# Optimization experiments

Measured on AMD Instinct MI355X. Metric: run time of the kernel, lower is better.

Reference implementation:

```python
import jax, jax.numpy as jnp
import numpy as np

B, IN, H, OUT, E = 4096, 1024, 2048, 1024, 16

def setup_inputs() -> dict:
    key = jax.random.key(0)
    ks = jax.random.split(key, 8)
    def lin_init(k, shape, fan_in):
        bound = 1.0 / np.sqrt(fan_in)
        return jax.random.uniform(k, shape, jnp.float32, -bound, bound)
    return {
        "obs": jax.random.normal(ks[0], (B, IN), jnp.float32),
        "switch_idx": jax.random.randint(ks[1], (B,), 0, E, jnp.int32),
        "pre_w": lin_init(ks[2], (H, IN), IN),
        "pre_b": lin_init(ks[3], (H,), IN),
        "expert_w": lin_init(ks[4], (E, H, H), H),
        "expert_b": lin_init(ks[5], (E, H), H),
        "post_w": lin_init(ks[6], (OUT, H), H),
        "post_b": lin_init(ks[7], (OUT,), H),
    }

def reference(obs, switch_idx, pre_w, pre_b, expert_w, expert_b, post_w, post_b):
    # pre_switch: Linear + Tanh
    x = jnp.tanh(obs @ pre_w.T + pre_b)                      # [B, H]
    # compute ALL switch experts (faithful to torch.stack over switches)
    all_x = jnp.einsum("bi,eoi->beo", x, expert_w) + expert_b  # [B, E, H]
    # gather the selected expert output per sample
    x = jnp.take_along_axis(all_x, switch_idx[:, None, None].astype(jnp.int32), axis=1)[:, 0]  # [B, H]
    # post_switch: Tanh, Linear, Tanh
    x = jnp.tanh(x)
    return jnp.tanh(x @ post_w.T + post_b)                   # [B, OUT]
```

## Files before the change

### kernel.cpp

```cpp
#include <hip/hip_runtime.h>


#define Bsz 4096
#define INd 1024
#define Hd  2048
#define OUTd 1024
#define NEXP 16

#define BM 128
#define BN 128
#define BK 32
#define LDT 56

typedef short bf16x8 __attribute__((ext_vector_type(8)));
typedef float f32x4 __attribute__((ext_vector_type(4)));
typedef unsigned short u16;

__device__ __forceinline__ u16 f2bf(float f) {
  unsigned u = __float_as_uint(f);
  u += 0x7FFF + ((u >> 16) & 1);
  return (u16)(u >> 16);
}

__device__ __forceinline__ float fast_tanh(float x) {
  float ax = fabsf(x);
  float e = __expf(2.0f * ax);
  float t = 1.0f - 2.0f / (e + 1.0f);
  return x < 0.0f ? -t : t;
}

__device__ __forceinline__ void mfma_step(const u16* As, const u16* Bs,
                                          int wm, int wn, int fr, int fk,
                                          f32x4 acc[4][4]) {
  bf16x8 af[4], bq[4];
#pragma unroll
  for (int i = 0; i < 4; ++i) af[i] = *(const bf16x8*)&As[(wm + 16 * i + fr) * LDT + fk];
#pragma unroll
  for (int j = 0; j < 4; ++j) bq[j] = *(const bf16x8*)&Bs[(wn + 16 * j + fr) * LDT + fk];
#pragma unroll
  for (int i = 0; i < 4; ++i)
#pragma unroll
    for (int j = 0; j < 4; ++j)
      acc[i][j] = __builtin_amdgcn_mfma_f32_16x16x32_bf16(af[i], bq[j], acc[i][j], 0, 0, 0);
}

__global__ __launch_bounds__(256) void k_bucket(const int* __restrict__ idx,
                                                int* __restrict__ offs,
                                                int* __restrict__ rows) {
  __shared__ int cnt[NEXP];
  __shared__ int base[NEXP];
  int t = threadIdx.x;
  if (t < NEXP) cnt[t] = 0;
  __syncthreads();
  for (int b = t; b < Bsz; b += 256) atomicAdd(&cnt[idx[b]], 1);
  __syncthreads();
  if (t == 0) {
    int s = 0;
    for (int e = 0; e < NEXP; ++e) { base[e] = s; offs[e] = s; s += cnt[e]; }
    offs[NEXP] = s;
  }
  __syncthreads();
  for (int b = t; b < Bsz; b += 256) {
    int e = idx[b];
    int p = atomicAdd(&base[e], 1);
    rows[p] = b;
  }
}

__global__ __launch_bounds__(256) void k_pre(const float* __restrict__ obs,
                                             const float* __restrict__ pre_w,
                                             const float* __restrict__ pre_b,
                                             u16* __restrict__ X1) {
  __shared__ u16 As[BM * LDT];
  __shared__ u16 Bs[BN * LDT];
  const int n0 = blockIdx.x * BN;
  const int m0 = blockIdx.y * BM;
  const int tid = threadIdx.x;
  const int lane = tid & 63;
  const int wv = tid >> 6;
  const int wm = (wv >> 1) * 64, wn = (wv & 1) * 64;
  const int fr = lane & 15, fq = lane >> 4;
  const int fk = fq * 8;
  const int sr = tid >> 3;
  const int skc = (tid & 7) * 4;

  f32x4 acc[4][4] = {};

  for (int k0 = 0; k0 < INd; k0 += BK) {
#pragma unroll
    for (int p = 0; p < 4; ++p) {
      int row = sr + 32 * p;
      float4 va = *(const float4*)&obs[(size_t)(m0 + row) * INd + k0 + skc];
      ushort4 ha; ha.x = f2bf(va.x); ha.y = f2bf(va.y); ha.z = f2bf(va.z); ha.w = f2bf(va.w);
      *(ushort4*)&As[row * LDT + skc] = ha;
      float4 vb = *(const float4*)&pre_w[(size_t)(n0 + row) * INd + k0 + skc];
      ushort4 hb; hb.x = f2bf(vb.x); hb.y = f2bf(vb.y); hb.z = f2bf(vb.z); hb.w = f2bf(vb.w);
      *(ushort4*)&Bs[row * LDT + skc] = hb;
    }
    __syncthreads();
    mfma_step(As, Bs, wm, wn, fr, fk, acc);
    __syncthreads();
  }
#pragma unroll
  for (int j = 0; j < 4; ++j) {
    int col = n0 + wn + 16 * j + fr;
    float bias = pre_b[col];
#pragma unroll
    for (int i = 0; i < 4; ++i) {
      int rb = m0 + wm + 16 * i + fq * 4;
#pragma unroll
      for (int r = 0; r < 4; ++r)
        X1[(size_t)(rb + r) * Hd + col] = f2bf(fast_tanh(acc[i][j][r] + bias));
    }
  }
}

__global__ __launch_bounds__(256) void k_expert(const u16* __restrict__ X1,
                                                const float* __restrict__ ew,
                                                const float* __restrict__ eb,
                                                const int* __restrict__ offs,
                                                const int* __restrict__ rows,
                                                u16* __restrict__ Z) {
  __shared__ u16 As[BM * LDT];
  __shared__ u16 Bs[BN * LDT];
  const int e = blockIdx.y >> 5;
  const int rt = blockIdx.y & 31;
  const int seg = offs[e];
  const int cnt = offs[e + 1] - seg;
  const int tbase = rt * BM;
  if (tbase >= cnt) return;
  const int nval = min(BM, cnt - tbase);
  const int n0 = blockIdx.x * BN;
  const float* We = ew + (size_t)e * Hd * Hd;

  const int tid = threadIdx.x;
  const int lane = tid & 63;
  const int wv = tid >> 6;
  const int wm = (wv >> 1) * 64, wn = (wv & 1) * 64;
  const int fr = lane & 15, fq = lane >> 4;
  const int fk = fq * 8;

  const int ar_ = tid >> 2;
  const int akc = (tid & 3) * 8;
  int rowg[2];
#pragma unroll
  for (int p = 0; p < 2; ++p) {
    int ar = ar_ + 64 * p;
    rowg[p] = (ar < nval) ? rows[seg + tbase + ar] : -1;
  }
  const int sr = tid >> 3;
  const int skc = (tid & 7) * 4;

  f32x4 acc[4][4] = {};
  const float4 zero4 = {0.f, 0.f, 0.f, 0.f};

  for (int k0 = 0; k0 < Hd; k0 += BK) {
#pragma unroll
    for (int p = 0; p < 2; ++p) {
      int ar = ar_ + 64 * p;
      float4 v = (rowg[p] >= 0) ? *(const float4*)&X1[(size_t)rowg[p] * Hd + k0 + akc] : zero4;
      *(float4*)&As[ar * LDT + akc] = v;
    }
#pragma unroll
    for (int p = 0; p < 4; ++p) {
      int row = sr + 32 * p;
      float4 vb = *(const float4*)&We[(size_t)(n0 + row) * Hd + k0 + skc];
      ushort4 hb; hb.x = f2bf(vb.x); hb.y = f2bf(vb.y); hb.z = f2bf(vb.z); hb.w = f2bf(vb.w);
      *(ushort4*)&Bs[row * LDT + skc] = hb;
    }
    __syncthreads();
    mfma_step(As, Bs, wm, wn, fr, fk, acc);
    __syncthreads();
  }
#pragma unroll
  for (int i = 0; i < 4; ++i) {
#pragma unroll
    for (int r = 0; r < 4; ++r) {
      int arow = wm + 16 * i + fq * 4 + r;
      if (arow < nval) {
        int orow = rows[seg + tbase + arow];
#pragma unroll
        for (int j = 0; j < 4; ++j) {
          int col = n0 + wn + 16 * j + fr;
          float bias = eb[(size_t)e * Hd + col];
          Z[(size_t)orow * Hd + col] = f2bf(fast_tanh(acc[i][j][r] + bias));
        }
      }
    }
  }
}

__global__ __launch_bounds__(256) void k_post(const u16* __restrict__ Z,
                                              const float* __restrict__ pw,
                                              const float* __restrict__ pb,
                                              float* __restrict__ out) {
  __shared__ u16 As[BM * LDT];
  __shared__ u16 Bs[BN * LDT];
  const int n0 = blockIdx.x * BN;
  const int m0 = blockIdx.y * BM;
  const int tid = threadIdx.x;
  const int lane = tid & 63;
  const int wv = tid >> 6;
  const int wm = (wv >> 1) * 64, wn = (wv & 1) * 64;
  const int fr = lane & 15, fq = lane >> 4;
  const int fk = fq * 8;
  const int ar_ = tid >> 2;
  const int akc = (tid & 3) * 8;
  const int sr = tid >> 3;
  const int skc = (tid & 7) * 4;

  f32x4 acc[4][4] = {};

  for (int k0 = 0; k0 < Hd; k0 += BK) {
#pragma unroll
    for (int p = 0; p < 2; ++p) {
      int ar = ar_ + 64 * p;
      float4 v = *(const float4*)&Z[(size_t)(m0 + ar) * Hd + k0 + akc];
      *(float4*)&As[ar * LDT + akc] = v;
    }
#pragma unroll
    for (int p = 0; p < 4; ++p) {
      int row = sr + 32 * p;
      float4 vb = *(const float4*)&pw[(size_t)(n0 + row) * Hd + k0 + skc];
      ushort4 hb; hb.x = f2bf(vb.x); hb.y = f2bf(vb.y); hb.z = f2bf(vb.z); hb.w = f2bf(vb.w);
      *(ushort4*)&Bs[row * LDT + skc] = hb;
    }
    __syncthreads();
    mfma_step(As, Bs, wm, wn, fr, fk, acc);
    __syncthreads();
  }
#pragma unroll
  for (int j = 0; j < 4; ++j) {
    int col = n0 + wn + 16 * j + fr;
    float bias = pb[col];
#pragma unroll
    for (int i = 0; i < 4; ++i) {
      int rb = m0 + wm + 16 * i + fq * 4;
#pragma unroll
      for (int r = 0; r < 4; ++r)
        out[(size_t)(rb + r) * OUTd + col] = fast_tanh(acc[i][j][r] + bias);
    }
  }
}

extern "C" void kernel_launch(void* const* d_in, const int* in_sizes, int n_in,
                              void* d_out, int out_size, void* d_ws, size_t ws_size,
                              hipStream_t stream) {
  const float* obs   = (const float*)d_in[0];
  const int*   sw    = (const int*)d_in[1];
  const float* pre_w = (const float*)d_in[2];
  const float* pre_b = (const float*)d_in[3];
  const float* ew    = (const float*)d_in[4];
  const float* eb    = (const float*)d_in[5];
  const float* pw    = (const float*)d_in[6];
  const float* pb    = (const float*)d_in[7];
  float* out = (float*)d_out;

  char* ws = (char*)d_ws;
  u16* X1   = (u16*)ws;
  u16* Z    = (u16*)(ws + (size_t)Bsz * Hd * 2);
  int* offs = (int*)(ws + (size_t)2 * Bsz * Hd * 2);
  int* rows = offs + 32;

  k_bucket<<<dim3(1), dim3(256), 0, stream>>>(sw, offs, rows);
  k_pre<<<dim3(Hd / BN, Bsz / BM), dim3(256), 0, stream>>>(obs, pre_w, pre_b, X1);
  k_expert<<<dim3(Hd / BN, NEXP * 32), dim3(256), 0, stream>>>(X1, ew, eb, offs, rows, Z);
  k_post<<<dim3(OUTd / BN, Bsz / BM), dim3(256), 0, stream>>>(Z, pw, pb, out);
}
```

Measured before the change: 649.6 us.

## Rewrite GEMM pipeline with bf16 pre-conversion, direct-to-LDS loads and double buffering

Adds conversion kernels that turn obs and the weights into bf16 in workspace, so the GEMMs stream bf16 through global_load_lds into XOR-swizzled, double-buffered LDS tiles with BK=64. A register-prefetch fallback runs when the workspace is too small. The post GEMM moves to 64-row tiles for more blocks. This removes per-tile fp32-to-bf16 conversion from the inner loops and overlaps loads with MFMA, at the cost of extra conversion passes over all weights (including 256MB of expert weights) on every call.

```diff
diff --git a/kernel.cpp b/kernel.cpp
--- a/kernel.cpp
+++ b/kernel.cpp
@@ -7,11 +7,6 @@
 #define OUTd 1024
 #define NEXP 16
 
-#define BM 128
-#define BN 128
-#define BK 32
-#define LDT 56
-
 typedef short bf16x8 __attribute__((ext_vector_type(8)));
 typedef float f32x4 __attribute__((ext_vector_type(4)));
 typedef unsigned short u16;
@@ -29,27 +24,88 @@
   return x < 0.0f ? -t : t;
 }
 
-__device__ __forceinline__ void mfma_step(const u16* As, const u16* Bs,
-                                          int wm, int wn, int fr, int fk,
-                                          f32x4 acc[4][4]) {
-  bf16x8 af[4], bq[4];
-#pragma unroll
-  for (int i = 0; i < 4; ++i) af[i] = *(const bf16x8*)&As[(wm + 16 * i + fr) * LDT + fk];
-#pragma unroll
-  for (int j = 0; j < 4; ++j) bq[j] = *(const bf16x8*)&Bs[(wn + 16 * j + fr) * LDT + fk];
-#pragma unroll
-  for (int i = 0; i < 4; ++i)
-#pragma unroll
-    for (int j = 0; j < 4; ++j)
-      acc[i][j] = __builtin_amdgcn_mfma_f32_16x16x32_bf16(af[i], bq[j], acc[i][j], 0, 0, 0);
+#define GLL16(g, l)                                                            \
+  __builtin_amdgcn_global_load_lds(                                            \
+      (const __attribute__((address_space(1))) unsigned int*)(g),              \
+      (__attribute__((address_space(3))) unsigned int*)(l), 16, 0, 0)
+
+__device__ __forceinline__ void stage128(const u16* gbase, int ldk, u16* lds, int t) {
+  const int row = t >> 3;
+  const int gc8 = ((t & 7) ^ (row & 7)) << 3;
+#pragma unroll
+  for (int p = 0; p < 4; ++p)
+    GLL16(gbase + (size_t)(row + 32 * p) * ldk + gc8, lds + ((t + 256 * p) << 3));
+}
+
+__device__ __forceinline__ void stage64(const u16* gbase, int ldk, u16* lds, int t) {
+  const int row = t >> 3;
+  const int gc8 = ((t & 7) ^ (row & 7)) << 3;
+#pragma unroll
+  for (int p = 0; p < 2; ++p)
+    GLL16(gbase + (size_t)(row + 32 * p) * ldk + gc8, lds + ((t + 256 * p) << 3));
+}
+
+__device__ __forceinline__ void stage_gather(const u16* X1k, const int rowg[4],
+                                             const u16* zeroc, u16* lds, int t) {
+  const int gc8 = ((t & 7) ^ ((t >> 3) & 7)) << 3;
+#pragma unroll
+  for (int p = 0; p < 4; ++p) {
+    const u16* g = (rowg[p] >= 0) ? X1k + (size_t)rowg[p] * Hd + gc8 : zeroc;
+    GLL16(g, lds + ((t + 256 * p) << 3));
+  }
+}
+
+struct F32Tile { float4 v[8]; };
+__device__ __forceinline__ void loadF32tile(const float* W, int ldk, int t, F32Tile& r) {
+  const int brow = t & 127, half = t >> 7;
+  const float* p = W + (size_t)brow * ldk + (half << 5);
+#pragma unroll
+  for (int q = 0; q < 8; ++q) r.v[q] = *(const float4*)(p + 4 * q);
+}
+__device__ __forceinline__ void writeF32tile(const F32Tile& r, u16* lds, int t) {
+  const int brow = t & 127, half = t >> 7;
+#pragma unroll
+  for (int q2 = 0; q2 < 4; ++q2) {
+    const float4 x = r.v[2 * q2], y = r.v[2 * q2 + 1];
+    bf16x8 o;
+    o[0] = (short)f2bf(x.x); o[1] = (short)f2bf(x.y);
+    o[2] = (short)f2bf(x.z); o[3] = (short)f2bf(x.w);
+    o[4] = (short)f2bf(y.x); o[5] = (short)f2bf(y.y);
+    o[6] = (short)f2bf(y.z); o[7] = (short)f2bf(y.w);
+    const int gq = (half << 2) + q2;
+    const int c = gq ^ (brow & 7);
+    *(bf16x8*)&lds[brow * 64 + (c << 3)] = o;
+  }
+}
+
+template <int MI>
+__device__ __forceinline__ void compute_tile(const u16* As, const u16* Bs,
+                                             int wm, int wn, int fr, int fq,
+                                             f32x4 (&acc)[MI][4]) {
+#pragma unroll
+  for (int ks = 0; ks < 2; ++ks) {
+    const int ch = (((ks << 2) + fq) ^ (fr & 7)) << 3;
+    bf16x8 af[MI], bq[4];
+#pragma unroll
+    for (int i = 0; i < MI; ++i) af[i] = *(const bf16x8*)&As[(wm + 16 * i + fr) * 64 + ch];
+#pragma unroll
+    for (int j = 0; j < 4; ++j) bq[j] = *(const bf16x8*)&Bs[(wn + 16 * j + fr) * 64 + ch];
+#pragma unroll
+    for (int i = 0; i < MI; ++i)
+#pragma unroll
+      for (int j = 0; j < 4; ++j)
+        acc[i][j] = __builtin_amdgcn_mfma_f32_16x16x32_bf16(af[i], bq[j], acc[i][j], 0, 0, 0);
+  }
 }
 
 __global__ __launch_bounds__(256) void k_bucket(const int* __restrict__ idx,
                                                 int* __restrict__ offs,
-                                                int* __restrict__ rows) {
+                                                int* __restrict__ rows,
+                                                int* __restrict__ zc) {
   __shared__ int cnt[NEXP];
   __shared__ int base[NEXP];
   int t = threadIdx.x;
+  if (t < 16) zc[t] = 0;
   if (t < NEXP) cnt[t] = 0;
   __syncthreads();
   for (int b = t; b < Bsz; b += 256) atomicAdd(&cnt[idx[b]], 1);
@@ -67,111 +123,155 @@
   }
 }
 
-__global__ __launch_bounds__(256) void k_pre(const float* __restrict__ obs,
-                                             const float* __restrict__ pre_w,
-                                             const float* __restrict__ pre_b,
-                                             u16* __restrict__ X1) {
-  __shared__ u16 As[BM * LDT];
-  __shared__ u16 Bs[BN * LDT];
-  const int n0 = blockIdx.x * BN;
-  const int m0 = blockIdx.y * BM;
-  const int tid = threadIdx.x;
-  const int lane = tid & 63;
-  const int wv = tid >> 6;
-  const int wm = (wv >> 1) * 64, wn = (wv & 1) * 64;
+__global__ __launch_bounds__(256) void k_cvt(const float* __restrict__ src,
+                                             u16* __restrict__ dst, int n) {
+  int i = (blockIdx.x * 256 + threadIdx.x) * 8;
+  if (i >= n) return;
+  float4 a = *(const float4*)(src + i);
+  float4 b = *(const float4*)(src + i + 4);
+  bf16x8 o;
+  o[0] = (short)f2bf(a.x); o[1] = (short)f2bf(a.y);
+  o[2] = (short)f2bf(a.z); o[3] = (short)f2bf(a.w);
+  o[4] = (short)f2bf(b.x); o[5] = (short)f2bf(b.y);
+  o[6] = (short)f2bf(b.z); o[7] = (short)f2bf(b.w);
+  *(bf16x8*)(dst + i) = o;
+}
+
+template <bool PC>
+__global__ __launch_bounds__(256) void k_pre_t(const float* __restrict__ obs32,
+                                               const u16* __restrict__ obsb,
+                                               const float* __restrict__ prew32,
+                                               const u16* __restrict__ prewb,
+                                               const float* __restrict__ pre_b,
+                                               u16* __restrict__ X1) {
+  __shared__ u16 As[2][128 * 64];
+  __shared__ u16 Bs[2][128 * 64];
+  const int tid = threadIdx.x, lane = tid & 63, wv = tid >> 6;
+  const int wm = (wv >> 1) << 6, wn = (wv & 1) << 6;
   const int fr = lane & 15, fq = lane >> 4;
-  const int fk = fq * 8;
-  const int sr = tid >> 3;
-  const int skc = (tid & 7) * 4;
-
+  const int n0 = blockIdx.x * 128, m0 = blockIdx.y * 128;
   f32x4 acc[4][4] = {};
-
-  for (int k0 = 0; k0 < INd; k0 += BK) {
-#pragma unroll
-    for (int p = 0; p < 4; ++p) {
-      int row = sr + 32 * p;
-      float4 va = *(const float4*)&obs[(size_t)(m0 + row) * INd + k0 + skc];
-      ushort4 ha; ha.x = f2bf(va.x); ha.y = f2bf(va.y); ha.z = f2bf(va.z); ha.w = f2bf(va.w);
-      *(ushort4*)&As[row * LDT + skc] = ha;
-      float4 vb = *(const float4*)&pre_w[(size_t)(n0 + row) * INd + k0 + skc];
-      ushort4 hb; hb.x = f2bf(vb.x); hb.y = f2bf(vb.y); hb.z = f2bf(vb.z); hb.w = f2bf(vb.w);
-      *(ushort4*)&Bs[row * LDT + skc] = hb;
-    }
-    __syncthreads();
-    mfma_step(As, Bs, wm, wn, fr, fk, acc);
-    __syncthreads();
-  }
+  const int NT = INd / 64;
+
+  if constexpr (PC) {
+    stage128(obsb + (size_t)m0 * INd, INd, As[0], tid);
+    stage128(prewb + (size_t)n0 * INd, INd, Bs[0], tid);
+    __syncthreads();
+    for (int kt = 0; kt < NT; ++kt) {
+      const int nb = (kt + 1) & 1;
+      if (kt + 1 < NT) {
+        stage128(obsb + (size_t)m0 * INd + (kt + 1) * 64, INd, As[nb], tid);
+        stage128(prewb + (size_t)n0 * INd + (kt + 1) * 64, INd, Bs[nb], tid);
+      }
+      compute_tile<4>(As[kt & 1], Bs[kt & 1], wm, wn, fr, fq, acc);
+      __syncthreads();
+    }
+  } else {
+    F32Tile ra, rb;
+    loadF32tile(obs32 + (size_t)m0 * INd, INd, tid, ra);
+    loadF32tile(prew32 + (size_t)n0 * INd, INd, tid, rb);
+    writeF32tile(ra, As[0], tid);
+    writeF32tile(rb, Bs[0], tid);
+    __syncthreads();
+    for (int kt = 0; kt < NT; ++kt) {
+      const int nb = (kt + 1) & 1;
+      const bool more = (kt + 1) < NT;
+      F32Tile na, nbv;
+      if (more) {
+        loadF32tile(obs32 + (size_t)m0 * INd + (kt + 1) * 64, INd, tid, na);
+        loadF32tile(prew32 + (size_t)n0 * INd + (kt + 1) * 64, INd, tid, nbv);
+      }
+      compute_tile<4>(As[kt & 1], Bs[kt & 1], wm, wn, fr, fq, acc);
+      if (more) { writeF32tile(na, As[nb], tid); writeF32tile(nbv, Bs[nb], tid); }
+      __syncthreads();
+    }
+  }
+
 #pragma unroll
   for (int j = 0; j < 4; ++j) {
     int col = n0 + wn + 16 * j + fr;
     float bias = pre_b[col];
 #pragma unroll
     for (int i = 0; i < 4; ++i) {
-      int rb = m0 + wm + 16 * i + fq * 4;
+      int rb2 = m0 + wm + 16 * i + fq * 4;
 #pragma unroll
       for (int r = 0; r < 4; ++r)
-        X1[(size_t)(rb + r) * Hd + col] = f2bf(fast_tanh(acc[i][j][r] + bias));
-    }
-  }
-}
-
-__global__ __launch_bounds__(256) void k_expert(const u16* __restrict__ X1,
-                                                const float* __restrict__ ew,
-                                                const float* __restrict__ eb,
-                                                const int* __restrict__ offs,
-                                                const int* __restrict__ rows,
-                                                u16* __restrict__ Z) {
-  __shared__ u16 As[BM * LDT];
-  __shared__ u16 Bs[BN * LDT];
-  const int e = blockIdx.y >> 5;
-  const int rt = blockIdx.y & 31;
-  const int seg = offs[e];
-  const int cnt = offs[e + 1] - seg;
-  const int tbase = rt * BM;
+        X1[(size_t)(rb2 + r) * Hd + col] = f2bf(fast_tanh(acc[i][j][r] + bias));
+    }
+  }
+}
+
+template <bool PC>
+__global__ __launch_bounds__(256) void k_expert_t(const u16* __restrict__ X1,
+                                                  const float* __restrict__ ew32,
+                                                  const u16* __restrict__ ewb,
+                                                  const float* __restrict__ eb,
+                                                  const int* __restrict__ offs,
+                                                  const int* __restrict__ rows,
+                                                  const u16* __restrict__ zeroc,
+                                                  u16* __restrict__ Z) {
+  const int e = blockIdx.y >> 5, rt = blockIdx.y & 31;
+  const int seg = offs[e], cnt = offs[e + 1] - seg;
+  const int tbase = rt * 128;
   if (tbase >= cnt) return;
-  const int nval = min(BM, cnt - tbase);
-  const int n0 = blockIdx.x * BN;
-  const float* We = ew + (size_t)e * Hd * Hd;
-
-  const int tid = threadIdx.x;
-  const int lane = tid & 63;
-  const int wv = tid >> 6;
-  const int wm = (wv >> 1) * 64, wn = (wv & 1) * 64;
+  const int nval = min(128, cnt - tbase);
+  const int n0 = blockIdx.x * 128;
+
+  __shared__ u16 As[2][128 * 64];
+  __shared__ u16 Bs[2][128 * 64];
+  const int tid = threadIdx.x, lane = tid & 63, wv = tid >> 6;
+  const int wm = (wv >> 1) << 6, wn = (wv & 1) << 6;
   const int fr = lane & 15, fq = lane >> 4;
-  const int fk = fq * 8;
-
-  const int ar_ = tid >> 2;
-  const int akc = (tid & 3) * 8;
-  int rowg[2];
-#pragma unroll
-  for (int p = 0; p < 2; ++p) {
-    int ar = ar_ + 64 * p;
-    rowg[p] = (ar < nval) ? rows[seg + tbase + ar] : -1;
-  }
-  const int sr = tid >> 3;
-  const int skc = (tid & 7) * 4;
-
+
+  int rowg[4];
+  {
+    const int r0 = tid >> 3;
+#pragma unroll
+    for (int p = 0; p < 4; ++p) {
+      int ar = r0 + 32 * p;
+      rowg[p] = (ar < nval) ? rows[seg + tbase + ar] : -1;
+    }
+  }
   f32x4 acc[4][4] = {};
-  const float4 zero4 = {0.f, 0.f, 0.f, 0.f};
-
-  for (int k0 = 0; k0 < Hd; k0 += BK) {
-#pragma unroll
-    for (int p = 0; p < 2; ++p) {
-      int ar = ar_ + 64 * p;
-      float4 v = (rowg[p] >= 0) ? *(const float4*)&X1[(size_t)rowg[p] * Hd + k0 + akc] : zero4;
-      *(float4*)&As[ar * LDT + akc] = v;
-    }
-#pragma unroll
-    for (int p = 0; p < 4; ++p) {
-      int row = sr + 32 * p;
-      float4 vb = *(const float4*)&We[(size_t)(n0 + row) * Hd + k0 + skc];
-      ushort4 hb; hb.x = f2bf(vb.x); hb.y = f2bf(vb.y); hb.z = f2bf(vb.z); hb.w = f2bf(vb.w);
-      *(ushort4*)&Bs[row * LDT + skc] = hb;
-    }
-    __syncthreads();
-    mfma_step(As, Bs, wm, wn, fr, fk, acc);
-    __syncthreads();
-  }
+  const int NT = Hd / 64;
+
+  if constexpr (PC) {
+    const u16* We = ewb + (size_t)e * Hd * Hd + (size_t)n0 * Hd;
+    stage_gather(X1, rowg, zeroc, As[0], tid);
+    stage128(We, Hd, Bs[0], tid);
+    __syncthreads();
+    for (int kt = 0; kt < NT; ++kt) {
+      const int nb = (kt + 1) & 1;
+      if (kt + 1 < NT) {
+        stage_gather(X1 + (kt + 1) * 64, rowg, zeroc, As[nb], tid);
+        stage128(We + (kt + 1) * 64, Hd, Bs[nb], tid);
+      }
+      compute_tile<4>(As[kt & 1], Bs[kt & 1], wm, wn, fr, fq, acc);
+      __syncthreads();
+    }
+  } else {
+    const float* We32 = ew32 + (size_t)e * Hd * Hd + (size_t)n0 * Hd;
+    stage_gather(X1, rowg, zeroc, As[0], tid);
+    {
+      F32Tile rb;
+      loadF32tile(We32, Hd, tid, rb);
+      writeF32tile(rb, Bs[0], tid);
+    }
+    __syncthreads();
+    for (int kt = 0; kt < NT; ++kt) {
+      const int nb = (kt + 1) & 1;
+      const bool more = (kt + 1) < NT;
+      F32Tile rn;
+      if (more) {
+        stage_gather(X1 + (kt + 1) * 64, rowg, zeroc, As[nb], tid);
+        loadF32tile(We32 + (kt + 1) * 64, Hd, tid, rn);
+      }
+      compute_tile<4>(As[kt & 1], Bs[kt & 1], wm, wn, fr, fq, acc);
+      if (more) writeF32tile(rn, Bs[nb], tid);
+      __syncthreads();
+    }
+  }
+
 #pragma unroll
   for (int i = 0; i < 4; ++i) {
 #pragma unroll
@@ -190,55 +290,66 @@
   }
 }
 
-__global__ __launch_bounds__(256) void k_post(const u16* __restrict__ Z,
-                                              const float* __restrict__ pw,
-                                              const float* __restrict__ pb,
-                                              float* __restrict__ out) {
-  __shared__ u16 As[BM * LDT];
-  __shared__ u16 Bs[BN * LDT];
-  const int n0 = blockIdx.x * BN;
-  const int m0 = blockIdx.y * BM;
-  const int tid = threadIdx.x;
-  const int lane = tid & 63;
-  const int wv = tid >> 6;
-  const int wm = (wv >> 1) * 64, wn = (wv & 1) * 64;
+template <bool PC>
+__global__ __launch_bounds__(256) void k_post_t(const u16* __restrict__ Z,
+                                                const float* __restrict__ pw32,
+                                                const u16* __restrict__ pwb,
+                                                const float* __restrict__ pb,
+                                                float* __restrict__ out) {
+  __shared__ u16 As[2][64 * 64];
+  __shared__ u16 Bs[2][128 * 64];
+  const int tid = threadIdx.x, lane = tid & 63, wv = tid >> 6;
+  const int wm = (wv >> 1) << 5, wn = (wv & 1) << 6;
   const int fr = lane & 15, fq = lane >> 4;
-  const int fk = fq * 8;
-  const int ar_ = tid >> 2;
-  const int akc = (tid & 3) * 8;
-  const int sr = tid >> 3;
-  const int skc = (tid & 7) * 4;
-
-  f32x4 acc[4][4] = {};
-
-  for (int k0 = 0; k0 < Hd; k0 += BK) {
-#pragma unroll
-    for (int p = 0; p < 2; ++p) {
-      int ar = ar_ + 64 * p;
-      float4 v = *(const float4*)&Z[(size_t)(m0 + ar) * Hd + k0 + akc];
-      *(float4*)&As[ar * LDT + akc] = v;
-    }
-#pragma unroll
-    for (int p = 0; p < 4; ++p) {
-      int row = sr + 32 * p;
-      float4 vb = *(const float4*)&pw[(size_t)(n0 + row) * Hd + k0 + skc];
-      ushort4 hb; hb.x = f2bf(vb.x); hb.y = f2bf(vb.y); hb.z = f2bf(vb.z); hb.w = f2bf(vb.w);
-      *(ushort4*)&Bs[row * LDT + skc] = hb;
-    }
-    __syncthreads();
-    mfma_step(As, Bs, wm, wn, fr, fk, acc);
-    __syncthreads();
-  }
+  const int n0 = blockIdx.x * 128, m0 = blockIdx.y * 64;
+  f32x4 acc[2][4] = {};
+  const int NT = Hd / 64;
+
+  if constexpr (PC) {
+    stage64(Z + (size_t)m0 * Hd, Hd, As[0], tid);
+    stage128(pwb + (size_t)n0 * Hd, Hd, Bs[0], tid);
+    __syncthreads();
+    for (int kt = 0; kt < NT; ++kt) {
+      const int nb = (kt + 1) & 1;
+      if (kt + 1 < NT) {
+        stage64(Z + (size_t)m0 * Hd + (kt + 1) * 64, Hd, As[nb], tid);
+        stage128(pwb + (size_t)n0 * Hd + (kt + 1) * 64, Hd, Bs[nb], tid);
+      }
+      compute_tile<2>(As[kt & 1], Bs[kt & 1], wm, wn, fr, fq, acc);
+      __syncthreads();
+    }
+  } else {
+    stage64(Z + (size_t)m0 * Hd, Hd, As[0], tid);
+    {
+      F32Tile rb;
+      loadF32tile(pw32 + (size_t)n0 * Hd, Hd, tid, rb);
+      writeF32tile(rb, Bs[0], tid);
+    }
+    __syncthreads();
+    for (int kt = 0; kt < NT; ++kt) {
+      const int nb = (kt + 1) & 1;
+      const bool more = (kt + 1) < NT;
+      F32Tile rn;
+      if (more) {
+        stage64(Z + (size_t)m0 * Hd + (kt + 1) * 64, Hd, As[nb], tid);
+        loadF32tile(pw32 + (size_t)n0 * Hd + (kt + 1) * 64, Hd, tid, rn);
+      }
+      compute_tile<2>(As[kt & 1], Bs[kt & 1], wm, wn, fr, fq, acc);
+      if (more) writeF32tile(rn, Bs[nb], tid);
+      __syncthreads();
+    }
+  }
+
 #pragma unroll
   for (int j = 0; j < 4; ++j) {
     int col = n0 + wn + 16 * j + fr;
     float bias = pb[col];
 #pragma unroll
-    for (int i = 0; i < 4; ++i) {
-      int rb = m0 + wm + 16 * i + fq * 4;
+    for (int i = 0; i < 2; ++i) {
+      int rb2 = m0 + wm + 16 * i + fq * 4;
 #pragma unroll
       for (int r = 0; r < 4; ++r)
-        out[(size_t)(rb + r) * OUTd + col] = fast_tanh(acc[i][j][r] + bias);
+        out[(size_t)(rb2 + r) * OUTd + col] = fast_tanh(acc[i][j][r] + bias);
     }
   }
 }
@@ -257,13 +368,43 @@
   float* out = (float*)d_out;
 
   char* ws = (char*)d_ws;
-  u16* X1   = (u16*)ws;
-  u16* Z    = (u16*)(ws + (size_t)Bsz * Hd * 2);
-  int* offs = (int*)(ws + (size_t)2 * Bsz * Hd * 2);
-  int* rows = offs + 32;
-
-  k_bucket<<<dim3(1), dim3(256), 0, stream>>>(sw, offs, rows);
-  k_pre<<<dim3(Hd / BN, Bsz / BM), dim3(256), 0, stream>>>(obs, pre_w, pre_b, X1);
-  k_expert<<<dim3(Hd / BN, NEXP * 32), dim3(256), 0, stream>>>(X1, ew, eb, offs, rows, Z);
-  k_post<<<dim3(OUTd / BN, Bsz / BM), dim3(256), 0, stream>>>(Z, pw, pb, out);
-}
+  int* offs = (int*)ws;
+  int* rows = (int*)(ws + 128);
+  u16* zeroc = (u16*)(ws + 128 + 16384);
+  const size_t MISC = 65536;
+  u16* X1     = (u16*)(ws + MISC);
+  u16* Zb     = (u16*)(ws + MISC + ((size_t)16 << 20));
+  u16* obsb   = (u16*)(ws + MISC + ((size_t)32 << 20));
+  u16* prewb  = (u16*)(ws + MISC + ((size_t)40 << 20));
+  u16* postwb = (u16*)(ws + MISC + ((size_t)44 << 20));
+  u16* ewb    = (u16*)(ws + MISC + ((size_t)48 << 20));
+  const size_t needMid  = MISC + ((size_t)48 << 20);
+  const size_t needFull = needMid + ((size_t)128 << 20);
+  const bool full = ws_size >= needFull;
+  const bool mid  = ws_size >= needMid;
+
+  k_bucket<<<dim3(1), dim3(256), 0, stream>>>(sw, offs, rows, (int*)zeroc);
+
+  if (mid) {
+    k_cvt<<<dim3(Bsz * INd / 2048), dim3(256), 0, stream>>>(obs, obsb, Bsz * INd);
+    k_cvt<<<dim3(Hd * INd / 2048), dim3(256), 0, stream>>>(pre_w, prewb, Hd * INd);
+    k_cvt<<<dim3(OUTd * Hd / 2048), dim3(256), 0, stream>>>(pw, postwb, OUTd * Hd);
+  }
+  if (full)
+    k_cvt<<<dim3(NEXP * Hd * Hd / 2048), dim3(256), 0, stream>>>(ew, ewb, NEXP * Hd * Hd);
+
+  if (mid)
+    k_pre_t<true><<<dim3(Hd / 128, Bsz / 128), dim3(256), 0, stream>>>(obs, obsb, pre_w, prewb, pre_b, X1);
+  else
+    k_pre_t<false><<<dim3(Hd / 128, Bsz / 128), dim3(256), 0, stream>>>(obs, obsb, pre_w, prewb, pre_b, X1);
+
+  if (full)
+    k_expert_t<true><<<dim3(Hd / 128, NEXP * 32), dim3(256), 0, stream>>>(X1, ew, ewb, eb, offs, rows, zeroc, Zb);
+  else
+    k_expert_t<false><<<dim3(Hd / 128, NEXP * 32), dim3(256), 0, stream>>>(X1, ew, ewb, eb, offs, rows, zeroc, Zb);
+
+  if (mid)
+    k_post_t<true><<<dim3(OUTd / 128, Bsz / 64), dim3(256), 0, stream>>>(Zb, pw, postwb, pb, out);
+  else
+    k_post_t<false><<<dim3(OUTd / 128, Bsz / 64), dim3(256), 0, stream>>>(Zb, pw, postwb, pb, out);
+}
```

Result: faster. 629.3 us (-3.1%).
